# Kernel tuning notes

Hardware: AMD Instinct MI355X
Metric: run time of the kernel (lower is better)

The kernel has to match this reference:

```python
import jax, jax.numpy as jnp
import numpy as np

B, S, DM = 2, 2048, 2048
H, KV, HD = 32, 8, 64
ROPE_BASE = 10000.0


def rotate_half(x):
    x1, x2 = jnp.split(x, 2, axis=-1)
    return jnp.concatenate([-x2, x1], axis=-1)


def setup_inputs() -> dict:
    key = jax.random.key(0)
    ks = jax.random.split(key, 8)
    hidden_states = jax.random.normal(ks[0], (B, S, DM), dtype=jnp.float32)
    attention_mask = jnp.ones((B, S), dtype=jnp.int32)
    # RoPE tables: inv_freq over half the head dim, duplicated (HF-style)
    inv_freq = 1.0 / (ROPE_BASE ** (jnp.arange(0, HD, 2, dtype=jnp.float32) / HD))
    pos = jnp.arange(S, dtype=jnp.float32)
    freqs = pos[:, None] * inv_freq[None, :]            # [S, HD/2]
    emb = jnp.concatenate([freqs, freqs], axis=-1)      # [S, HD]
    cos = jnp.broadcast_to(jnp.cos(emb)[None], (B, S, HD))
    sin = jnp.broadcast_to(jnp.sin(emb)[None], (B, S, HD))
    sc = 1.0 / np.sqrt(DM)
    W_q = jax.random.normal(ks[1], (DM, H * HD), dtype=jnp.float32) * sc
    W_k = jax.random.normal(ks[2], (DM, KV * HD), dtype=jnp.float32) * sc
    W_v = jax.random.normal(ks[3], (DM, KV * HD), dtype=jnp.float32) * sc
    b_v = jax.random.normal(ks[4], (KV * HD,), dtype=jnp.float32) * 0.01
    W_o = jax.random.normal(ks[5], (H * HD, DM), dtype=jnp.float32) * sc
    b_o = jax.random.normal(ks[6], (DM,), dtype=jnp.float32) * 0.01
    return {"hidden_states": hidden_states, "attention_mask": attention_mask,
            "cos": cos, "sin": sin, "W_q": W_q, "W_k": W_k, "W_v": W_v,
            "b_v": b_v, "W_o": W_o, "b_o": b_o}


def reference(hidden_states, attention_mask, cos, sin, W_q, W_k, W_v, b_v, W_o, b_o):
    b, s, _ = hidden_states.shape
    q = hidden_states @ W_q                       # [B,S,H*HD]
    k = hidden_states @ W_k                       # [B,S,KV*HD]
    v = hidden_states @ W_v + b_v                 # [B,S,KV*HD]
    q = q.reshape(b, s, H, HD).transpose(0, 2, 1, 3)    # [B,H,S,HD]
    k = k.reshape(b, s, KV, HD).transpose(0, 2, 1, 3)   # [B,KV,S,HD]
    v = v.reshape(b, s, KV, HD).transpose(0, 2, 1, 3)
    c = cos[:, None]                              # [B,1,S,HD]
    sn = sin[:, None]
    q = q * c + rotate_half(q) * sn
    k = k * c + rotate_half(k) * sn
    groups = H // KV
    k = jnp.repeat(k, groups, axis=1)             # [B,H,S,HD]
    v = jnp.repeat(v, groups, axis=1)
    A = jnp.einsum('bhqd,bhkd->bhqk', q, k) / np.sqrt(HD).astype(np.float32)
    neg_inf = jnp.float32(-jnp.inf)
    causal = jnp.triu(jnp.full((s, s), neg_inf, dtype=jnp.float32), k=1)[None, None]
    mask = jnp.where(attention_mask[:, None, None, :] == 0, neg_inf, causal)
    A = jax.nn.softmax(A + mask, axis=-1)
    o = jnp.einsum('bhqk,bhkd->bhqd', A, v)
    o = o.transpose(0, 2, 1, 3).reshape(b, s, H * HD)
    return o @ W_o + b_o
```

## Files before the change

kernel.cpp:

```cpp
#include <hip/hip_runtime.h>
#include <hip/hip_bf16.h>

#define Bb 2
#define Ss 2048
#define DMD 2048
#define Hh 32
#define KVh 8
#define HD 64

using bf16 = __hip_bfloat16;
typedef __attribute__((ext_vector_type(8))) short short8;
typedef __attribute__((ext_vector_type(4))) float floatx4;

__device__ inline float tof(const bf16 x) { return __bfloat162float(x); }
__device__ inline void stor(float* p, float v) { *p = v; }
__device__ inline void stor(bf16* p, float v) { *p = __float2bfloat16(v); }
__device__ inline short bf16bits(float v) {
    union { bf16 h; short s; } cv; cv.h = __float2bfloat16(v); return cv.s;
}

__device__ inline void gl_lds16(const bf16* g, bf16* l) {
    __builtin_amdgcn_global_load_lds(
        (const __attribute__((address_space(1))) unsigned int*)g,
        (__attribute__((address_space(3))) unsigned int*)l, 16, 0, 0);
}

__global__ __launch_bounds__(256) void cvt_bf16_kernel(
    const float* __restrict__ in, bf16* __restrict__ out, int total8)
{
    const int i = blockIdx.x * 256 + threadIdx.x;
    if (i >= total8) return;
    const float4 a = ((const float4*)in)[2 * i];
    const float4 b = ((const float4*)in)[2 * i + 1];
    short8 r;
    r[0] = bf16bits(a.x); r[1] = bf16bits(a.y); r[2] = bf16bits(a.z); r[3] = bf16bits(a.w);
    r[4] = bf16bits(b.x); r[5] = bf16bits(b.y); r[6] = bf16bits(b.z); r[7] = bf16bits(b.w);
    ((short8*)out)[i] = r;
}

__global__ __launch_bounds__(256) void cvtT_kernel(
    const float* __restrict__ W, bf16* __restrict__ Wt,
    int N, int K, int rowOff)
{
    __shared__ float t[32][33];
    const int n0 = blockIdx.x * 32;
    const int k0 = blockIdx.y * 32;
    const int tx = threadIdx.x & 31, ty = threadIdx.x >> 5;
    #pragma unroll
    for (int r = 0; r < 32; r += 8)
        t[ty + r][tx] = W[(size_t)(k0 + ty + r) * N + n0 + tx];
    __syncthreads();
    #pragma unroll
    for (int r = 0; r < 32; r += 8)
        Wt[(size_t)(rowOff + n0 + ty + r) * K + k0 + tx] =
            __float2bfloat16(t[tx][ty + r]);
}

template <int EPI>
__global__ __launch_bounds__(256) void gemm_bt(
    const bf16* __restrict__ A, const bf16* __restrict__ Bt,
    const float* __restrict__ bias,
    bf16* __restrict__ Yq, bf16* __restrict__ Yk, bf16* __restrict__ Yv,
    float* __restrict__ Yo, int M, int N, int K)
{
    __shared__ bf16 As[128 * 32];
    __shared__ bf16 Bs[128 * 32];

    const int tid  = threadIdx.x;
    const int wave = tid >> 6, lane = tid & 63;
    const int lid  = lane & 15, quad = lane >> 4;
    const int wr = (wave >> 1) * 64, wc = (wave & 1) * 64;
    const size_t bm = (size_t)blockIdx.y * 128, bn = (size_t)blockIdx.x * 128;

    floatx4 acc[4][4];
    #pragma unroll
    for (int i = 0; i < 4; ++i)
        #pragma unroll
        for (int j = 0; j < 4; ++j)
            acc[i][j] = (floatx4){0.f, 0.f, 0.f, 0.f};

    for (int k0 = 0; k0 < K; k0 += 32) {
        #pragma unroll
        for (int i = 0; i < 2; ++i) {
            const int c   = wave * 128 + i * 64 + lane;
            const int row = c >> 2, col = (c & 3) * 8;
            gl_lds16(A  + (bm + row) * (size_t)K + k0 + col,
                     &As[(wave * 128 + i * 64) * 8]);
            gl_lds16(Bt + (bn + row) * (size_t)K + k0 + col,
                     &Bs[(wave * 128 + i * 64) * 8]);
        }
        __syncthreads();

        short8 af[4], bfr[4];
        #pragma unroll
        for (int i = 0; i < 4; ++i)
            af[i] = *(const short8*)&As[(wr + i * 16 + lid) * 32 + quad * 8];
        #pragma unroll
        for (int j = 0; j < 4; ++j)
            bfr[j] = *(const short8*)&Bs[(wc + j * 16 + lid) * 32 + quad * 8];
        #pragma unroll
        for (int i = 0; i < 4; ++i)
            #pragma unroll
            for (int j = 0; j < 4; ++j)
                acc[i][j] = __builtin_amdgcn_mfma_f32_16x16x32_bf16(
                    af[i], bfr[j], acc[i][j], 0, 0, 0);
        __syncthreads();
    }

    #pragma unroll
    for (int i = 0; i < 4; ++i) {
        const int gm0 = (int)bm + wr + i * 16 + quad * 4;
        #pragma unroll
        for (int j = 0; j < 4; ++j) {
            const int gn = (int)bn + wc + j * 16 + lid;
            #pragma unroll
            for (int r = 0; r < 4; ++r) {
                float v = acc[i][j][r];
                const int gm = gm0 + r;
                if (EPI == 0) {
                    if (gn < Hh * HD) {
                        stor(&Yq[(size_t)gm * (Hh * HD) + gn], v);
                    } else if (gn < Hh * HD + KVh * HD) {
                        stor(&Yk[(size_t)gm * (KVh * HD) + (gn - Hh * HD)], v);
                    } else {
                        const int c = gn - (Hh * HD + KVh * HD);
                        v += bias[c];
                        const int kvh = c >> 6, dd = c & 63;
                        const int bbi = gm >> 11, s = gm & (Ss - 1);
                        stor(&Yv[(((size_t)bbi * KVh + kvh) * HD + dd) * Ss + s], v);
                    }
                } else {
                    Yo[(size_t)gm * N + gn] = v + bias[gn];
                }
            }
        }
    }
}

__global__ void rope_kernel(bf16* __restrict__ buf,
                            const float* __restrict__ cosb,
                            const float* __restrict__ sinb,
                            int nheads, int total, float scale)
{
    int idx = blockIdx.x * blockDim.x + threadIdx.x;
    if (idx >= total) return;
    int d = idx & 31;
    int h = (idx >> 5) % nheads;
    int bs = idx / (32 * nheads);
    bf16* row = buf + ((size_t)bs * nheads + h) * HD;
    float x1 = tof(row[d]), x2 = tof(row[d + 32]);
    float c1 = cosb[(size_t)bs * HD + d];
    float s1 = sinb[(size_t)bs * HD + d];
    float c2 = cosb[(size_t)bs * HD + d + 32];
    float s2 = sinb[(size_t)bs * HD + d + 32];
    stor(&row[d],      (x1 * c1 - x2 * s1) * scale);
    stor(&row[d + 32], (x2 * c2 + x1 * s2) * scale);
}

template <bool CAUSAL>
__device__ inline void fattn_tile(
    const int k0, const int m0,
    const bf16* __restrict__ kBase, const bf16* __restrict__ vBase,
    const int* __restrict__ mBase,
    const short8 qf0[2], const short8 qf1[2],
    floatx4 o[2][4], float lsum[2][4],
    short (*pw)[16][72],
    const int lid, const int quad)
{
    const size_t kStride = (size_t)KVh * HD;

    short8 kb0[4], kb1[4];
    #pragma unroll
    for (int nt = 0; nt < 4; ++nt) {
        const bf16* kr = kBase + (size_t)(k0 + nt * 16 + lid) * kStride + quad * 8;
        kb0[nt] = *(const short8*)(kr);
        kb1[nt] = *(const short8*)(kr + 32);
    }
    floatx4 s[2][4];
    __builtin_amdgcn_s_setprio(1);
    #pragma unroll
    for (int nt = 0; nt < 4; ++nt)
        #pragma unroll
        for (int g = 0; g < 2; ++g) {
            floatx4 c = (floatx4){0.f, 0.f, 0.f, 0.f};
            c = __builtin_amdgcn_mfma_f32_16x16x32_bf16(qf0[g], kb0[nt], c, 0, 0, 0);
            c = __builtin_amdgcn_mfma_f32_16x16x32_bf16(qf1[g], kb1[nt], c, 0, 0, 0);
            s[g][nt] = c;
        }
    __builtin_amdgcn_s_setprio(0);

    short8 vb0[4], vb1[4];
    #pragma unroll
    for (int nt = 0; nt < 4; ++nt) {
        const bf16* vr = vBase + (size_t)(nt * 16 + lid) * Ss + k0 + quad * 8;
        vb0[nt] = *(const short8*)(vr);
        vb1[nt] = *(const short8*)(vr + 32);
    }

    #pragma unroll
    for (int nt = 0; nt < 4; ++nt) {
        const int col = k0 + nt * 16 + lid;
        const int mk  = mBase[col];
        #pragma unroll
        for (int g = 0; g < 2; ++g) {
            const int mr0 = m0 + g * 16 + quad * 4;
            #pragma unroll
            for (int rr = 0; rr < 4; ++rr) {
                float p;
                if (CAUSAL)
                    p = (mk == 0 || col > mr0 + rr) ? 0.f : __expf(s[g][nt][rr]);
                else
                    p = (mk == 0) ? 0.f : __expf(s[g][nt][rr]);
                s[g][nt][rr] = p;
                lsum[g][rr] += p;
            }
        }
    }

    #pragma unroll
    for (int g = 0; g < 2; ++g)
        #pragma unroll
        for (int nt = 0; nt < 4; ++nt)
            #pragma unroll
            for (int rr = 0; rr < 4; ++rr)
                pw[g][quad * 4 + rr][nt * 16 + lid] = bf16bits(s[g][nt][rr]);
    short8 pf0[2], pf1[2];
    #pragma unroll
    for (int g = 0; g < 2; ++g) {
        pf0[g] = *(const short8*)&pw[g][lid][quad * 8];
        pf1[g] = *(const short8*)&pw[g][lid][32 + quad * 8];
    }

    __builtin_amdgcn_s_setprio(1);
    #pragma unroll
    for (int nt = 0; nt < 4; ++nt)
        #pragma unroll
        for (int g = 0; g < 2; ++g) {
            o[g][nt] = __builtin_amdgcn_mfma_f32_16x16x32_bf16(
                pf0[g], vb0[nt], o[g][nt], 0, 0, 0);
            o[g][nt] = __builtin_amdgcn_mfma_f32_16x16x32_bf16(
                pf1[g], vb1[nt], o[g][nt], 0, 0, 0);
        }
    __builtin_amdgcn_s_setprio(0);
}

__global__ __launch_bounds__(256) void fattn_kernel(
    bf16* __restrict__ QO, const bf16* __restrict__ Kb,
    const bf16* __restrict__ Vt, const int* __restrict__ mask)
{
    const int bid    = blockIdx.x;
    const int kvh    = bid & 7;
    const int rest   = bid >> 3;
    const int qbslot = rest >> 3;
    const int bh     = rest & 7;
    const int hg     = bh & 3;
    const int b      = bh >> 2;
    const int qb     = 15 - qbslot;
    const int h      = kvh * 4 + hg;

    const int tid  = threadIdx.x;
    const int wave = tid >> 6;
    const int lane = tid & 63;
    const int lid  = lane & 15;
    const int quad = lane >> 4;

    const int qw = qb * 4 + wave;
    const int m0 = qw * 32;
    const int nfull = qw >> 1;

    __shared__ short pLds[4][2][16][72];

    const size_t kStride = (size_t)KVh * HD;
    const bf16* kBase = Kb + ((size_t)b * Ss) * kStride + (size_t)kvh * HD;
    const bf16* vBase = Vt + ((size_t)(b * KVh + kvh) * HD) * Ss;
    const int*  mBase = mask + b * Ss;

    short8 qf0[2], qf1[2];
    #pragma unroll
    for (int g = 0; g < 2; ++g) {
        const bf16* qb_ = QO + ((size_t)(b * Ss + m0 + g * 16 + lid) * Hh + h) * HD
                        + quad * 8;
        qf0[g] = *(const short8*)(qb_);
        qf1[g] = *(const short8*)(qb_ + 32);
    }

    floatx4 o[2][4];
    float lsum[2][4];
    #pragma unroll
    for (int g = 0; g < 2; ++g) {
        #pragma unroll
        for (int nt = 0; nt < 4; ++nt) o[g][nt] = (floatx4){0.f, 0.f, 0.f, 0.f};
        #pragma unroll
        for (int rr = 0; rr < 4; ++rr) lsum[g][rr] = 0.f;
    }

    for (int kt = 0; kt < nfull; ++kt)
        fattn_tile<false>(kt * 64, m0, kBase, vBase, mBase,
                          qf0, qf1, o, lsum, pLds[wave], lid, quad);
    fattn_tile<true>(nfull * 64, m0, kBase, vBase, mBase,
                     qf0, qf1, o, lsum, pLds[wave], lid, quad);

    #pragma unroll
    for (int g = 0; g < 2; ++g)
        #pragma unroll
        for (int rr = 0; rr < 4; ++rr) {
            float rs = lsum[g][rr];
            rs += __shfl_xor(rs, 1);
            rs += __shfl_xor(rs, 2);
            rs += __shfl_xor(rs, 4);
            rs += __shfl_xor(rs, 8);
            const float inv = 1.f / rs;
            const int m = m0 + g * 16 + quad * 4 + rr;
            bf16* orow = QO + ((size_t)(b * Ss + m) * Hh + h) * HD;
            #pragma unroll
            for (int nt = 0; nt < 4; ++nt)
                stor(&orow[nt * 16 + lid], o[g][nt][rr] * inv);
        }
}

extern "C" void kernel_launch(void* const* d_in, const int* in_sizes, int n_in,
                              void* d_out, int out_size, void* d_ws, size_t ws_size,
                              hipStream_t stream)
{
    const float* hs   = (const float*)d_in[0];
    const int*   mask = (const int*)d_in[1];
    const float* cosb = (const float*)d_in[2];
    const float* sinb = (const float*)d_in[3];
    const float* Wq   = (const float*)d_in[4];
    const float* Wk   = (const float*)d_in[5];
    const float* Wv   = (const float*)d_in[6];
    const float* bv   = (const float*)d_in[7];
    const float* Wo   = (const float*)d_in[8];
    const float* bo   = (const float*)d_in[9];
    float* out = (float*)d_out;

    const int M = Bb * Ss;

    bf16* QO    = (bf16*)d_ws;
    bf16* Wqkvt = QO + (size_t)M * (Hh * HD);
    bf16* Wot   = Wqkvt + (size_t)3072 * DMD;

    bf16* Kb  = (bf16*)d_out;
    bf16* Vt  = Kb + (size_t)M * (KVh * HD);
    bf16* Abf = Vt + (size_t)M * (KVh * HD);

    dim3 blk(256);

    const int total8 = M * DMD / 8;
    cvt_bf16_kernel<<<(total8 + 255) / 256, blk, 0, stream>>>(hs, Abf, total8);
    cvtT_kernel<<<dim3((Hh * HD) / 32, DMD / 32), blk, 0, stream>>>(
        Wq, Wqkvt, Hh * HD, DMD, 0);
    cvtT_kernel<<<dim3((KVh * HD) / 32, DMD / 32), blk, 0, stream>>>(
        Wk, Wqkvt, KVh * HD, DMD, Hh * HD);
    cvtT_kernel<<<dim3((KVh * HD) / 32, DMD / 32), blk, 0, stream>>>(
        Wv, Wqkvt, KVh * HD, DMD, Hh * HD + KVh * HD);
    cvtT_kernel<<<dim3(DMD / 32, DMD / 32), blk, 0, stream>>>(
        Wo, Wot, DMD, DMD, 0);

    gemm_bt<0><<<dim3(3072 / 128, M / 128), blk, 0, stream>>>(
        Abf, Wqkvt, bv, QO, Kb, Vt, nullptr, M, 3072, DMD);

    int totq = M * Hh * 32, totk = M * KVh * 32;
    rope_kernel<<<(totq + 255) / 256, blk, 0, stream>>>(QO, cosb, sinb, Hh, totq, 0.125f);
    rope_kernel<<<(totk + 255) / 256, blk, 0, stream>>>(Kb, cosb, sinb, KVh, totk, 1.0f);

    fattn_kernel<<<dim3(1024), blk, 0, stream>>>(QO, Kb, Vt, mask);

    gemm_bt<1><<<dim3(DMD / 128, M / 128), blk, 0, stream>>>(
        QO, Wot, bo, nullptr, nullptr, nullptr, out, M, DMD, DMD);
}
```

Measured before the change: 411.4 us.

## Fuse RoPE into QKV GEMM epilogue, merge weight transposes, widen attention tiles

The four weight-transpose launches become one kernel. The two RoPE kernels are removed by applying rotary embedding and the Q scale inside the QKV GEMM epilogue, so Q and K no longer make an extra round trip through memory. The flash-attention kernel now gives each wave 64 query rows instead of 32, halving the grid and reusing each K/V load across more rows. It also reorders the query-block schedule to balance causal work. The larger per-wave tile raises register pressure and may lower occupancy.

```diff
diff --git a/kernel.cpp b/kernel.cpp
--- a/kernel.cpp
+++ b/kernel.cpp
@@ -38,13 +38,20 @@
     ((short8*)out)[i] = r;
 }
 
-__global__ __launch_bounds__(256) void cvtT_kernel(
-    const float* __restrict__ W, bf16* __restrict__ Wt,
-    int N, int K, int rowOff)
+__global__ __launch_bounds__(256) void cvtT_all_kernel(
+    const float* __restrict__ Wq, const float* __restrict__ Wk,
+    const float* __restrict__ Wv, const float* __restrict__ Wo,
+    bf16* __restrict__ Wqkvt, bf16* __restrict__ Wot)
 {
     __shared__ float t[32][33];
-    const int n0 = blockIdx.x * 32;
+    const int nc = blockIdx.x * 32;
     const int k0 = blockIdx.y * 32;
+    const float* W; int N, n0, dstRow; bf16* dst;
+    if (nc < 2048)      { W = Wq; N = 2048; n0 = nc;        dst = Wqkvt; dstRow = nc; }
+    else if (nc < 2560) { W = Wk; N = 512;  n0 = nc - 2048; dst = Wqkvt; dstRow = nc; }
+    else if (nc < 3072) { W = Wv; N = 512;  n0 = nc - 2560; dst = Wqkvt; dstRow = nc; }
+    else                { W = Wo; N = 2048; n0 = nc - 3072; dst = Wot;   dstRow = nc - 3072; }
+
     const int tx = threadIdx.x & 31, ty = threadIdx.x >> 5;
     #pragma unroll
     for (int r = 0; r < 32; r += 8)
@@ -52,7 +59,7 @@
     __syncthreads();
     #pragma unroll
     for (int r = 0; r < 32; r += 8)
-        Wt[(size_t)(rowOff + n0 + ty + r) * K + k0 + tx] =
+        dst[(size_t)(dstRow + ty + r) * DMD + k0 + tx] =
             __float2bfloat16(t[tx][ty + r]);
 }
 
@@ -60,6 +67,7 @@
 __global__ __launch_bounds__(256) void gemm_bt(
     const bf16* __restrict__ A, const bf16* __restrict__ Bt,
     const float* __restrict__ bias,
+    const float* __restrict__ cosb, const float* __restrict__ sinb,
     bf16* __restrict__ Yq, bf16* __restrict__ Yk, bf16* __restrict__ Yv,
     float* __restrict__ Yo, int M, int N, int K)
 {
@@ -107,64 +115,82 @@
         __syncthreads();
     }
 
-    #pragma unroll
-    for (int i = 0; i < 4; ++i) {
-        const int gm0 = (int)bm + wr + i * 16 + quad * 4;
-        #pragma unroll
-        for (int j = 0; j < 4; ++j) {
-            const int gn = (int)bn + wc + j * 16 + lid;
-            #pragma unroll
-            for (int r = 0; r < 4; ++r) {
-                float v = acc[i][j][r];
-                const int gm = gm0 + r;
-                if (EPI == 0) {
-                    if (gn < Hh * HD) {
-                        stor(&Yq[(size_t)gm * (Hh * HD) + gn], v);
-                    } else if (gn < Hh * HD + KVh * HD) {
-                        stor(&Yk[(size_t)gm * (KVh * HD) + (gn - Hh * HD)], v);
-                    } else {
-                        const int c = gn - (Hh * HD + KVh * HD);
-                        v += bias[c];
-                        const int kvh = c >> 6, dd = c & 63;
+    if (EPI == 0) {
+        const int colbase = (int)bn + wc;
+        if (colbase < Hh * HD + KVh * HD) {
+            const bool isQ = colbase < Hh * HD;
+            const float scale = isQ ? 0.125f : 1.0f;
+            #pragma unroll
+            for (int i = 0; i < 4; ++i) {
+                const int gm0 = (int)bm + wr + i * 16 + quad * 4;
+                #pragma unroll
+                for (int r = 0; r < 4; ++r) {
+                    const int gm = gm0 + r;
+                    const float* crow = cosb + (size_t)gm * HD;
+                    const float* srow = sinb + (size_t)gm * HD;
+                    #pragma unroll
+                    for (int jp = 0; jp < 2; ++jp) {
+                        const int d1 = jp * 16 + lid;
+                        const float x1 = acc[i][jp][r];
+                        const float x2 = acc[i][jp + 2][r];
+                        const float c1 = crow[d1],      s1 = srow[d1];
+                        const float c2 = crow[d1 + 32], s2 = srow[d1 + 32];
+                        const float y1 = (x1 * c1 - x2 * s1) * scale;
+                        const float y2 = (x2 * c2 + x1 * s2) * scale;
+                        const int gn1 = colbase + d1;
+                        if (isQ) {
+                            stor(&Yq[(size_t)gm * (Hh * HD) + gn1],      y1);
+                            stor(&Yq[(size_t)gm * (Hh * HD) + gn1 + 32], y2);
+                        } else {
+                            const int cK = gn1 - Hh * HD;
+                            stor(&Yk[(size_t)gm * (KVh * HD) + cK],      y1);
+                            stor(&Yk[(size_t)gm * (KVh * HD) + cK + 32], y2);
+                        }
+                    }
+                }
+            }
+        } else {
+            #pragma unroll
+            for (int i = 0; i < 4; ++i) {
+                const int gm0 = (int)bm + wr + i * 16 + quad * 4;
+                #pragma unroll
+                for (int j = 0; j < 4; ++j) {
+                    const int gn = colbase + j * 16 + lid;
+                    const int c  = gn - (Hh * HD + KVh * HD);
+                    const int kvh = c >> 6, dd = c & 63;
+                    #pragma unroll
+                    for (int r = 0; r < 4; ++r) {
+                        const float v = acc[i][j][r] + bias[c];
+                        const int gm = gm0 + r;
                         const int bbi = gm >> 11, s = gm & (Ss - 1);
                         stor(&Yv[(((size_t)bbi * KVh + kvh) * HD + dd) * Ss + s], v);
                     }
-                } else {
-                    Yo[(size_t)gm * N + gn] = v + bias[gn];
                 }
             }
         }
-    }
-}
-
-__global__ void rope_kernel(bf16* __restrict__ buf,
-                            const float* __restrict__ cosb,
-                            const float* __restrict__ sinb,
-                            int nheads, int total, float scale)
-{
-    int idx = blockIdx.x * blockDim.x + threadIdx.x;
-    if (idx >= total) return;
-    int d = idx & 31;
-    int h = (idx >> 5) % nheads;
-    int bs = idx / (32 * nheads);
-    bf16* row = buf + ((size_t)bs * nheads + h) * HD;
-    float x1 = tof(row[d]), x2 = tof(row[d + 32]);
-    float c1 = cosb[(size_t)bs * HD + d];
-    float s1 = sinb[(size_t)bs * HD + d];
-    float c2 = cosb[(size_t)bs * HD + d + 32];
-    float s2 = sinb[(size_t)bs * HD + d + 32];
-    stor(&row[d],      (x1 * c1 - x2 * s1) * scale);
-    stor(&row[d + 32], (x2 * c2 + x1 * s2) * scale);
+    } else {
+        #pragma unroll
+        for (int i = 0; i < 4; ++i) {
+            const int gm0 = (int)bm + wr + i * 16 + quad * 4;
+            #pragma unroll
+            for (int j = 0; j < 4; ++j) {
+                const int gn = (int)bn + wc + j * 16 + lid;
+                #pragma unroll
+                for (int r = 0; r < 4; ++r)
+                    Yo[(size_t)(gm0 + r) * N + gn] = acc[i][j][r] + bias[gn];
+            }
+        }
+    }
 }
 
 template <bool CAUSAL>
-__device__ inline void fattn_tile(
+__device__ __forceinline__ void fattn_tile64(
     const int k0, const int m0,
     const bf16* __restrict__ kBase, const bf16* __restrict__ vBase,
     const int* __restrict__ mBase,
-    const short8 qf0[2], const short8 qf1[2],
-    floatx4 o[2][4], float lsum[2][4],
-    short (*pw)[16][72],
+    const short8 qf0[4], const short8 qf1[4],
+    floatx4 o[4][4], float lsum[4][4],
+    short (*pw)[16][76],
     const int lid, const int quad)
 {
     const size_t kStride = (size_t)KVh * HD;
@@ -176,19 +202,6 @@
         kb0[nt] = *(const short8*)(kr);
         kb1[nt] = *(const short8*)(kr + 32);
     }
-    floatx4 s[2][4];
-    __builtin_amdgcn_s_setprio(1);
-    #pragma unroll
-    for (int nt = 0; nt < 4; ++nt)
-        #pragma unroll
-        for (int g = 0; g < 2; ++g) {
-            floatx4 c = (floatx4){0.f, 0.f, 0.f, 0.f};
-            c = __builtin_amdgcn_mfma_f32_16x16x32_bf16(qf0[g], kb0[nt], c, 0, 0, 0);
-            c = __builtin_amdgcn_mfma_f32_16x16x32_bf16(qf1[g], kb1[nt], c, 0, 0, 0);
-            s[g][nt] = c;
-        }
-    __builtin_amdgcn_s_setprio(0);
-
     short8 vb0[4], vb1[4];
     #pragma unroll
     for (int nt = 0; nt < 4; ++nt) {
@@ -196,67 +209,69 @@
         vb0[nt] = *(const short8*)(vr);
         vb1[nt] = *(const short8*)(vr + 32);
     }
-
-    #pragma unroll
-    for (int nt = 0; nt < 4; ++nt) {
-        const int col = k0 + nt * 16 + lid;
-        const int mk  = mBase[col];
-        #pragma unroll
-        for (int g = 0; g < 2; ++g) {
-            const int mr0 = m0 + g * 16 + quad * 4;
+    int mk[4];
+    #pragma unroll
+    for (int nt = 0; nt < 4; ++nt) mk[nt] = mBase[k0 + nt * 16 + lid];
+
+    #pragma unroll
+    for (int g = 0; g < 4; ++g) {
+        floatx4 s[4];
+        __builtin_amdgcn_s_setprio(1);
+        #pragma unroll
+        for (int nt = 0; nt < 4; ++nt) {
+            floatx4 c = (floatx4){0.f, 0.f, 0.f, 0.f};
+            c = __builtin_amdgcn_mfma_f32_16x16x32_bf16(qf0[g], kb0[nt], c, 0, 0, 0);
+            c = __builtin_amdgcn_mfma_f32_16x16x32_bf16(qf1[g], kb1[nt], c, 0, 0, 0);
+            s[nt] = c;
+        }
+        __builtin_amdgcn_s_setprio(0);
+        const int mr0 = m0 + g * 16 + quad * 4;
+        #pragma unroll
+        for (int nt = 0; nt < 4; ++nt) {
+            const int col = k0 + nt * 16 + lid;
             #pragma unroll
             for (int rr = 0; rr < 4; ++rr) {
                 float p;
                 if (CAUSAL)
-                    p = (mk == 0 || col > mr0 + rr) ? 0.f : __expf(s[g][nt][rr]);
+                    p = (mk[nt] == 0 || col > mr0 + rr) ? 0.f : __expf(s[nt][rr]);
                 else
-                    p = (mk == 0) ? 0.f : __expf(s[g][nt][rr]);
-                s[g][nt][rr] = p;
+                    p = (mk[nt] == 0) ? 0.f : __expf(s[nt][rr]);
                 lsum[g][rr] += p;
+                pw[g][quad * 4 + rr][nt * 16 + lid] = bf16bits(p);
             }
         }
     }
 
     #pragma unroll
-    for (int g = 0; g < 2; ++g)
-        #pragma unroll
-        for (int nt = 0; nt < 4; ++nt)
-            #pragma unroll
-            for (int rr = 0; rr < 4; ++rr)
-                pw[g][quad * 4 + rr][nt * 16 + lid] = bf16bits(s[g][nt][rr]);
-    short8 pf0[2], pf1[2];
-    #pragma unroll
-    for (int g = 0; g < 2; ++g) {
-        pf0[g] = *(const short8*)&pw[g][lid][quad * 8];
-        pf1[g] = *(const short8*)&pw[g][lid][32 + quad * 8];
-    }
-
-    __builtin_amdgcn_s_setprio(1);
-    #pragma unroll
-    for (int nt = 0; nt < 4; ++nt)
-        #pragma unroll
-        for (int g = 0; g < 2; ++g) {
+    for (int g = 0; g < 4; ++g) {
+        const short8 pf0 = *(const short8*)&pw[g][lid][quad * 8];
+        const short8 pf1 = *(const short8*)&pw[g][lid][32 + quad * 8];
+        __builtin_amdgcn_s_setprio(1);
+        #pragma unroll
+        for (int nt = 0; nt < 4; ++nt) {
             o[g][nt] = __builtin_amdgcn_mfma_f32_16x16x32_bf16(
-                pf0[g], vb0[nt], o[g][nt], 0, 0, 0);
+                pf0, vb0[nt], o[g][nt], 0, 0, 0);
             o[g][nt] = __builtin_amdgcn_mfma_f32_16x16x32_bf16(
-                pf1[g], vb1[nt], o[g][nt], 0, 0, 0);
-        }
-    __builtin_amdgcn_s_setprio(0);
+                pf1, vb1[nt], o[g][nt], 0, 0, 0);
+        }
+        __builtin_amdgcn_s_setprio(0);
+    }
 }
 
 __global__ __launch_bounds__(256) void fattn_kernel(
     bf16* __restrict__ QO, const bf16* __restrict__ Kb,
     const bf16* __restrict__ Vt, const int* __restrict__ mask)
 {
-    const int bid    = blockIdx.x;
-    const int kvh    = bid & 7;
-    const int rest   = bid >> 3;
-    const int qbslot = rest >> 3;
-    const int bh     = rest & 7;
-    const int hg     = bh & 3;
-    const int b      = bh >> 2;
-    const int qb     = 15 - qbslot;
-    const int h      = kvh * 4 + hg;
+    const int bid  = blockIdx.x;
+    const int kvh  = bid & 7;
+    const int rest = bid >> 3;
+    const int low  = rest & 31, half = rest >> 5;
+    const int bh   = low & 7;
+    const int q3   = low >> 3;
+    const int qb   = half ? (7 - 2 * q3) : (2 * q3);
+    const int hg   = bh & 3;
+    const int b    = bh >> 2;
+    const int h    = kvh * 4 + hg;
 
     const int tid  = threadIdx.x;
     const int wave = tid >> 6;
@@ -265,29 +280,29 @@
     const int quad = lane >> 4;
 
     const int qw = qb * 4 + wave;
-    const int m0 = qw * 32;
-    const int nfull = qw >> 1;
-
-    __shared__ short pLds[4][2][16][72];
+    const int m0 = qw * 64;
+    const int nfull = qw;
+
+    __shared__ short pLds[4][4][16][76];
 
     const size_t kStride = (size_t)KVh * HD;
     const bf16* kBase = Kb + ((size_t)b * Ss) * kStride + (size_t)kvh * HD;
     const bf16* vBase = Vt + ((size_t)(b * KVh + kvh) * HD) * Ss;
     const int*  mBase = mask + b * Ss;
 
-    short8 qf0[2], qf1[2];
-    #pragma unroll
-    for (int g = 0; g < 2; ++g) {
+    short8 qf0[4], qf1[4];
+    #pragma unroll
+    for (int g = 0; g < 4; ++g) {
         const bf16* qb_ = QO + ((size_t)(b * Ss + m0 + g * 16 + lid) * Hh + h) * HD
                         + quad * 8;
         qf0[g] = *(const short8*)(qb_);
         qf1[g] = *(const short8*)(qb_ + 32);
     }
 
-    floatx4 o[2][4];
-    float lsum[2][4];
-    #pragma unroll
-    for (int g = 0; g < 2; ++g) {
+    floatx4 o[4][4];
+    float lsum[4][4];
+    #pragma unroll
+    for (int g = 0; g < 4; ++g) {
         #pragma unroll
         for (int nt = 0; nt < 4; ++nt) o[g][nt] = (floatx4){0.f, 0.f, 0.f, 0.f};
         #pragma unroll
@@ -295,13 +310,13 @@
     }
 
     for (int kt = 0; kt < nfull; ++kt)
-        fattn_tile<false>(kt * 64, m0, kBase, vBase, mBase,
-                          qf0, qf1, o, lsum, pLds[wave], lid, quad);
-    fattn_tile<true>(nfull * 64, m0, kBase, vBase, mBase,
-                     qf0, qf1, o, lsum, pLds[wave], lid, quad);
-
-    #pragma unroll
-    for (int g = 0; g < 2; ++g)
+        fattn_tile64<false>(kt * 64, m0, kBase, vBase, mBase,
+                            qf0, qf1, o, lsum, pLds[wave], lid, quad);
+    fattn_tile64<true>(nfull * 64, m0, kBase, vBase, mBase,
+                       qf0, qf1, o, lsum, pLds[wave], lid, quad);
+
+    #pragma unroll
+    for (int g = 0; g < 4; ++g)
         #pragma unroll
         for (int rr = 0; rr < 4; ++rr) {
             float rs = lsum[g][rr];
@@ -348,24 +363,14 @@
 
     const int total8 = M * DMD / 8;
     cvt_bf16_kernel<<<(total8 + 255) / 256, blk, 0, stream>>>(hs, Abf, total8);
-    cvtT_kernel<<<dim3((Hh * HD) / 32, DMD / 32), blk, 0, stream>>>(
-        Wq, Wqkvt, Hh * HD, DMD, 0);
-    cvtT_kernel<<<dim3((KVh * HD) / 32, DMD / 32), blk, 0, stream>>>(
-        Wk, Wqkvt, KVh * HD, DMD, Hh * HD);
-    cvtT_kernel<<<dim3((KVh * HD) / 32, DMD / 32), blk, 0, stream>>>(
-        Wv, Wqkvt, KVh * HD, DMD, Hh * HD + KVh * HD);
-    cvtT_kernel<<<dim3(DMD / 32, DMD / 32), blk, 0, stream>>>(
-        Wo, Wot, DMD, DMD, 0);
+    cvtT_all_kernel<<<dim3(5120 / 32, DMD / 32), blk, 0, stream>>>(
+        Wq, Wk, Wv, Wo, Wqkvt, Wot);
 
     gemm_bt<0><<<dim3(3072 / 128, M / 128), blk, 0, stream>>>(
-        Abf, Wqkvt, bv, QO, Kb, Vt, nullptr, M, 3072, DMD);
-
-    int totq = M * Hh * 32, totk = M * KVh * 32;
-    rope_kernel<<<(totq + 255) / 256, blk, 0, stream>>>(QO, cosb, sinb, Hh, totq, 0.125f);
-    rope_kernel<<<(totk + 255) / 256, blk, 0, stream>>>(Kb, cosb, sinb, KVh, totk, 1.0f);
-
-    fattn_kernel<<<dim3(1024), blk, 0, stream>>>(QO, Kb, Vt, mask);
+        Abf, Wqkvt, bv, cosb, sinb, QO, Kb, Vt, nullptr, M, 3072, DMD);
+
+    fattn_kernel<<<dim3(512), blk, 0, stream>>>(QO, Kb, Vt, mask);
 
     gemm_bt<1><<<dim3(DMD / 128, M / 128), blk, 0, stream>>>(
-        QO, Wot, bo, nullptr, nullptr, nullptr, out, M, DMD, DMD);
-}
+        QO, Wot, bo, nullptr, nullptr, nullptr, nullptr, nullptr, out, M, DMD, DMD);
+}
```

New measurement: 360.3 us. 1.14x faster.
